# Optimization experiments

Measured on AMD Instinct MI355X. Metric: run time of the kernel, lower is better.

The kernel has to match this reference:

```python
import jax, jax.numpy as jnp
import numpy as np

B, P, K, HE, HF = 256, 128, 512, 1024, 512
D = K + HE + 2 * HF  # 2560, MLP input dim
HID = 64


def setup_inputs() -> dict:
    key = jax.random.key(0)
    ks = jax.random.split(key, 6)
    query = jax.random.normal(ks[0], (B, 1, HE), dtype=jnp.float32)
    keys = jax.random.normal(ks[1], (B, P, K), dtype=jnp.float32)
    frameLSTM_h = jax.random.normal(ks[2], (B, 1, 2 * HF), dtype=jnp.float32)
    mask = jax.random.randint(ks[3], (B, P), 0, 2, dtype=jnp.int32)
    mask = mask.at[:, 0].set(1)  # guarantee at least one unmasked player per row
    W1 = jax.random.normal(ks[4], (D, HID), dtype=jnp.float32) / np.float32(np.sqrt(D))
    W2 = jax.random.normal(ks[5], (HID, 1), dtype=jnp.float32) / np.float32(np.sqrt(HID))
    return dict(query=query, keys=keys, frameLSTM_h=frameLSTM_h, mask=mask, W1=W1, W2=W2)


def reference(query, keys, frameLSTM_h, mask, W1, W2):
    # Faithful to: cat([keys, query.repeat, frame.repeat]) @ W1 -> ReLU -> @ W2.
    # The pre-activation is linear, so splitting W1 by row-blocks is exactly the
    # same math without materializing the repeated/concatenated (B,P,D) tensor.
    W1k = W1[:K]            # (K, 64)
    W1q = W1[K:K + HE]      # (HE, 64)
    W1f = W1[K + HE:]       # (2*HF, 64)
    h = jax.nn.relu(
        jnp.einsum('bpk,kh->bph', keys, W1k)
        + jnp.einsum('boe,eh->boh', query, W1q)        # broadcasts over P
        + jnp.einsum('bof,fh->boh', frameLSTM_h, W1f)  # broadcasts over P
    )  # (B, P, 64)
    raw_scores = jnp.einsum('bph,ho->bp', h, W2)  # (B, P)
    raw_scores = jnp.where(mask == 0, -jnp.inf, raw_scores)
    weights = jax.nn.softmax(raw_scores, axis=1)  # (B, P)
    context = jnp.einsum('bp,bpk->bk', weights, keys)[:, None, :]  # (B, 1, K)
    embeddings = jnp.concatenate([context, frameLSTM_h], axis=2)   # (B, 1, K+2*HF)
    return embeddings, weights
```

## Files before the change

### kernel.cpp

```cpp
#include <hip/hip_runtime.h>
#include <hip/hip_bf16.h>
#include <cstdint>
#include <math.h>


typedef __bf16 bf16;
typedef __attribute__((ext_vector_type(8))) __bf16 bf16x8;
typedef __attribute__((ext_vector_type(4))) float f32x4;

#define NB 256
#define NP 128
#define NK 512

__global__ __launch_bounds__(512) void prep_kernel(
    const float* __restrict__ W1, const float* __restrict__ query,
    const float* __restrict__ frame, bf16* __restrict__ w1kt,
    float* __restrict__ proj)
{
    __shared__ float s[64][65];
    __shared__ float sq[4][2048];
    __shared__ float red[8][4][64];
    const int blk = blockIdx.x;
    const int t = threadIdx.x;
    if (blk < 8) {
        const int k0 = blk * 64;
#pragma unroll
        for (int i = 0; i < 8; i++) {
            const int idx = t + 512 * i;
            const int k = idx >> 6, h = idx & 63;
            s[k][h] = W1[(size_t)(k0 + k) * 64 + h];
        }
        __syncthreads();
#pragma unroll
        for (int i = 0; i < 8; i++) {
            const int idx = t + 512 * i;
            const int h = idx >> 6, kk = idx & 63;
            w1kt[(size_t)h * 512 + k0 + kk] = (bf16)s[kk][h];
        }
    } else {
        const int b0 = (blk - 8) * 4;
#pragma unroll
        for (int i = 0; i < 4; i++) {
            const int flat = (t + 512 * i) * 4;
            const int bl = flat >> 11;
            const int d  = flat & 2047;
            const float* src = (d < 1024)
                ? (query + (size_t)(b0 + bl) * 1024 + d)
                : (frame + (size_t)(b0 + bl) * 1024 + (d - 1024));
            *(float4*)&sq[bl][d] = *(const float4*)src;
        }
        __syncthreads();

        const int w = t >> 6;
        const int h = t & 63;
        const float* w1c = W1 + (size_t)(512 + w * 256) * 64 + h;
        float wreg[4][16];
#pragma unroll
        for (int bu = 0; bu < 3; bu++)
#pragma unroll
            for (int u = 0; u < 16; u++)
                wreg[bu][u] = w1c[(size_t)(bu * 16 + u) * 64];

        float acc[4] = {0.f, 0.f, 0.f, 0.f};
#pragma unroll
        for (int rr = 0; rr < 16; rr++) {
            const int cur = rr & 3;
            if (rr < 13) {
#pragma unroll
                for (int u = 0; u < 16; u++)
                    wreg[(rr + 3) & 3][u] = w1c[(size_t)((rr + 3) * 16 + u) * 64];
            }
#pragma unroll
            for (int u4 = 0; u4 < 4; u4++) {
                float4 qv[4];
#pragma unroll
                for (int j = 0; j < 4; j++)
                    qv[j] = *(const float4*)&sq[j][w * 256 + rr * 16 + u4 * 4];
#pragma unroll
                for (int uu = 0; uu < 4; uu++) {
                    const float wv = wreg[cur][u4 * 4 + uu];
                    acc[0] += (&qv[0].x)[uu] * wv;
                    acc[1] += (&qv[1].x)[uu] * wv;
                    acc[2] += (&qv[2].x)[uu] * wv;
                    acc[3] += (&qv[3].x)[uu] * wv;
                }
            }
        }
#pragma unroll
        for (int j = 0; j < 4; j++) red[w][j][h] = acc[j];
        __syncthreads();
        if (t < 256) {
            const int j2 = t >> 6, hh = t & 63;
            float sum = 0.f;
#pragma unroll
            for (int ww = 0; ww < 8; ww++) sum += red[ww][j2][hh];
            proj[(size_t)(b0 + j2) * 64 + hh] = sum;
        }
    }
}

__global__ __launch_bounds__(256) void scores_kernel(
    const float* __restrict__ keys, const float* __restrict__ W2,
    const bf16* __restrict__ w1kt, const float* __restrict__ proj,
    float* __restrict__ sws)
{
    extern __shared__ char sB[];
    const int blk = blockIdx.x;
    const int b = blk >> 1;
    const int ph = blk & 1;
    const int t = threadIdx.x;
    const int w = t >> 6;
    const int lane = t & 63;
    const int m = lane & 15;
    const int q = lane >> 4;
    const int p0 = ph * 64 + w * 16;
    const int xorv = (m & 7) << 4;

    const float* arow = keys + (size_t)b * (NP * NK) + (size_t)(p0 + m) * NK + q * 8;

    float4 Aa[4], Ab[4];
#pragma unroll
    for (int i = 0; i < 3; i++) {
        Aa[i] = *(const float4*)(arow + i * 32);
        Ab[i] = *(const float4*)(arow + i * 32 + 4);
    }

    {
        const char* wsrc = (const char*)w1kt;
#pragma unroll
        for (int i = 0; i < 16; i++) {
            const int o = t * 256 + i * 16;
            const int row = o >> 10;
            *(bf16x8*)(sB + (o ^ ((row & 7) << 4))) = *(const bf16x8*)(wsrc + o);
        }
    }

    float pv[4], wv[4];
#pragma unroll
    for (int nt = 0; nt < 4; nt++) {
        pv[nt] = proj[b * 64 + nt * 16 + m];
        wv[nt] = W2[nt * 16 + m];
    }
    __syncthreads();

    f32x4 acc[4];
#pragma unroll
    for (int nt = 0; nt < 4; nt++) acc[nt] = (f32x4){0.f, 0.f, 0.f, 0.f};

    bf16x8 Bp[2][4];
#pragma unroll
    for (int nt = 0; nt < 4; nt++)
        Bp[0][nt] = *(const bf16x8*)(sB + nt * 16384 + m * 1024 + ((q * 16) ^ xorv));

#pragma unroll
    for (int kk = 0; kk < 16; kk++) {
        const int cur = kk & 3;
        const int bc = kk & 1;
        if (kk < 13) {
            Aa[(kk + 3) & 3] = *(const float4*)(arow + (kk + 3) * 32);
            Ab[(kk + 3) & 3] = *(const float4*)(arow + (kk + 3) * 32 + 4);
        }
        if (kk < 15) {
#pragma unroll
            for (int nt = 0; nt < 4; nt++)
                Bp[bc ^ 1][nt] = *(const bf16x8*)(sB + nt * 16384 + m * 1024
                                  + ((((kk + 1) * 64) | (q * 16)) ^ xorv));
        }
        bf16x8 Af;
        Af[0] = (bf16)Aa[cur].x; Af[1] = (bf16)Aa[cur].y;
        Af[2] = (bf16)Aa[cur].z; Af[3] = (bf16)Aa[cur].w;
        Af[4] = (bf16)Ab[cur].x; Af[5] = (bf16)Ab[cur].y;
        Af[6] = (bf16)Ab[cur].z; Af[7] = (bf16)Ab[cur].w;
#pragma unroll
        for (int nt = 0; nt < 4; nt++)
            acc[nt] = __builtin_amdgcn_mfma_f32_16x16x32_bf16(Af, Bp[bc][nt], acc[nt], 0, 0, 0);
    }

    float pr[4] = {0.f, 0.f, 0.f, 0.f};
#pragma unroll
    for (int nt = 0; nt < 4; nt++)
#pragma unroll
        for (int r = 0; r < 4; r++)
            pr[r] += fmaxf(acc[nt][r] + pv[nt], 0.f) * wv[nt];

#pragma unroll
    for (int off = 1; off < 16; off <<= 1)
#pragma unroll
        for (int r = 0; r < 4; r++)
            pr[r] += __shfl_xor(pr[r], off);

    if (m == 0) {
#pragma unroll
        for (int r = 0; r < 4; r++)
            sws[(size_t)b * 128 + p0 + q * 4 + r] = pr[r];
    }
}

__global__ __launch_bounds__(512, 2) void ctx_kernel(
    const float* __restrict__ keys, const float* __restrict__ frame,
    const int* __restrict__ mask, const float* __restrict__ sws,
    float* __restrict__ out)
{
    __shared__ float wts[128];
    const int b = blockIdx.x;
    const int t = threadIdx.x;

    if (t < 64) {
        const int pa = t, pb = t + 64;
        float s0 = (mask[b * 128 + pa] == 0) ? -INFINITY : sws[(size_t)b * 128 + pa];
        float s1 = (mask[b * 128 + pb] == 0) ? -INFINITY : sws[(size_t)b * 128 + pb];
        float mx = fmaxf(s0, s1);
#pragma unroll
        for (int off = 32; off; off >>= 1) mx = fmaxf(mx, __shfl_xor(mx, off));
        float e0 = __expf(s0 - mx), e1 = __expf(s1 - mx);
        float sum = e0 + e1;
#pragma unroll
        for (int off = 32; off; off >>= 1) sum += __shfl_xor(sum, off);
        const float inv = 1.0f / sum;
        e0 *= inv; e1 *= inv;
        wts[pa] = e0; wts[pb] = e1;
        float* wout = out + (size_t)NB * 1536;
        wout[b * 128 + pa] = e0;
        wout[b * 128 + pb] = e1;
    }
    __syncthreads();

    const float* kc = keys + (size_t)b * (NP * NK) + t;
    float kreg[2][16];
#pragma unroll
    for (int i = 0; i < 16; i++) kreg[0][i] = kc[(size_t)i * NK];
    float acc = 0.f;
#pragma unroll
    for (int c8 = 0; c8 < 8; c8++) {
        const int cur = c8 & 1;
        if (c8 < 7) {
#pragma unroll
            for (int i = 0; i < 16; i++)
                kreg[cur ^ 1][i] = kc[(size_t)((c8 + 1) * 16 + i) * NK];
        }
#pragma unroll
        for (int i = 0; i < 16; i++)
            acc += wts[c8 * 16 + i] * kreg[cur][i];
    }
    out[(size_t)b * 1536 + t] = acc;

    if (t < 256) {
        const float4 fv = *(const float4*)(frame + (size_t)b * 1024 + t * 4);
        *(float4*)(out + (size_t)b * 1536 + 512 + t * 4) = fv;
    }
}

extern "C" void kernel_launch(void* const* d_in, const int* in_sizes, int n_in,
                              void* d_out, int out_size, void* d_ws, size_t ws_size,
                              hipStream_t stream) {
    const float* query = (const float*)d_in[0];
    const float* keys  = (const float*)d_in[1];
    const float* frame = (const float*)d_in[2];
    const int*   mask  = (const int*)d_in[3];
    const float* W1    = (const float*)d_in[4];
    const float* W2    = (const float*)d_in[5];
    float* out = (float*)d_out;

    bf16* w1kt  = (bf16*)d_ws;
    float* proj = (float*)((char*)d_ws + (64 << 10));
    float* sws  = (float*)((char*)d_ws + (128 << 10));

    hipFuncSetAttribute((const void*)scores_kernel,
                        hipFuncAttributeMaxDynamicSharedMemorySize, 65536);

    prep_kernel<<<72, 512, 0, stream>>>(W1, query, frame, w1kt, proj);
    scores_kernel<<<512, 256, 65536, stream>>>(keys, W2, w1kt, proj, sws);
    ctx_kernel<<<256, 512, 0, stream>>>(keys, frame, mask, sws, out);
}
```

Measured before the change: 130.6 us.

## Fuse scores and context kernels into one per-batch attention kernel

Merges the MFMA score kernel and the softmax/context kernel into a single kernel with one 512-thread block per batch row. Scores stay in shared memory instead of going through a global workspace, which removes one launch and the global round trip. The block also reads keys a second time while they may still be in L2. The key prefetch depth grows from 3 to 6 stages. The risks are that the grid drops to 256 blocks with more than 64KB of LDS each, which lowers occupancy and parallelism, and that the W1 tile load into LDS is now done once per batch rather than split across two blocks.

```diff
diff --git a/kernel.cpp b/kernel.cpp
--- a/kernel.cpp
+++ b/kernel.cpp
@@ -11,6 +11,7 @@
 #define NB 256
 #define NP 128
 #define NK 512
+#define SMEM_BYTES (65536 + 256 * 4)
 
 __global__ __launch_bounds__(512) void prep_kernel(
     const float* __restrict__ W1, const float* __restrict__ query,
@@ -99,28 +100,31 @@
     }
 }
 
-__global__ __launch_bounds__(256) void scores_kernel(
-    const float* __restrict__ keys, const float* __restrict__ W2,
+__global__ __launch_bounds__(512) void attn_kernel(
+    const float* __restrict__ keys, const float* __restrict__ frame,
+    const int* __restrict__ mask, const float* __restrict__ W2,
     const bf16* __restrict__ w1kt, const float* __restrict__ proj,
-    float* __restrict__ sws)
+    float* __restrict__ out)
 {
-    extern __shared__ char sB[];
-    const int blk = blockIdx.x;
-    const int b = blk >> 1;
-    const int ph = blk & 1;
+    extern __shared__ char smem[];
+    char* sB      = smem;
+    float* scores = (float*)(smem + 65536);
+    float* wts    = scores + 128;
+
+    const int b = blockIdx.x;
     const int t = threadIdx.x;
     const int w = t >> 6;
     const int lane = t & 63;
     const int m = lane & 15;
     const int q = lane >> 4;
-    const int p0 = ph * 64 + w * 16;
+    const int p0 = w * 16;
     const int xorv = (m & 7) << 4;
 
     const float* arow = keys + (size_t)b * (NP * NK) + (size_t)(p0 + m) * NK + q * 8;
 
-    float4 Aa[4], Ab[4];
-#pragma unroll
-    for (int i = 0; i < 3; i++) {
+    float4 Aa[8], Ab[8];
+#pragma unroll
+    for (int i = 0; i < 6; i++) {
         Aa[i] = *(const float4*)(arow + i * 32);
         Ab[i] = *(const float4*)(arow + i * 32 + 4);
     }
@@ -128,8 +132,8 @@
     {
         const char* wsrc = (const char*)w1kt;
 #pragma unroll
-        for (int i = 0; i < 16; i++) {
-            const int o = t * 256 + i * 16;
+        for (int i = 0; i < 8; i++) {
+            const int o = i * 8192 + t * 16;
             const int row = o >> 10;
             *(bf16x8*)(sB + (o ^ ((row & 7) << 4))) = *(const bf16x8*)(wsrc + o);
         }
@@ -154,11 +158,11 @@
 
 #pragma unroll
     for (int kk = 0; kk < 16; kk++) {
-        const int cur = kk & 3;
+        const int cur = kk & 7;
         const int bc = kk & 1;
-        if (kk < 13) {
-            Aa[(kk + 3) & 3] = *(const float4*)(arow + (kk + 3) * 32);
-            Ab[(kk + 3) & 3] = *(const float4*)(arow + (kk + 3) * 32 + 4);
+        if (kk < 10) {
+            Aa[(kk + 6) & 7] = *(const float4*)(arow + (kk + 6) * 32);
+            Ab[(kk + 6) & 7] = *(const float4*)(arow + (kk + 6) * 32 + 4);
         }
         if (kk < 15) {
 #pragma unroll
@@ -191,24 +195,14 @@
 
     if (m == 0) {
 #pragma unroll
-        for (int r = 0; r < 4; r++)
-            sws[(size_t)b * 128 + p0 + q * 4 + r] = pr[r];
-    }
-}
-
-__global__ __launch_bounds__(512, 2) void ctx_kernel(
-    const float* __restrict__ keys, const float* __restrict__ frame,
-    const int* __restrict__ mask, const float* __restrict__ sws,
-    float* __restrict__ out)
-{
-    __shared__ float wts[128];
-    const int b = blockIdx.x;
-    const int t = threadIdx.x;
+        for (int r = 0; r < 4; r++) scores[p0 + q * 4 + r] = pr[r];
+    }
+    __syncthreads();
 
     if (t < 64) {
         const int pa = t, pb = t + 64;
-        float s0 = (mask[b * 128 + pa] == 0) ? -INFINITY : sws[(size_t)b * 128 + pa];
-        float s1 = (mask[b * 128 + pb] == 0) ? -INFINITY : sws[(size_t)b * 128 + pb];
+        float s0 = (mask[b * 128 + pa] == 0) ? -INFINITY : scores[pa];
+        float s1 = (mask[b * 128 + pb] == 0) ? -INFINITY : scores[pb];
         float mx = fmaxf(s0, s1);
 #pragma unroll
         for (int off = 32; off; off >>= 1) mx = fmaxf(mx, __shfl_xor(mx, off));
@@ -225,25 +219,26 @@
     }
     __syncthreads();
 
-    const float* kc = keys + (size_t)b * (NP * NK) + t;
-    float kreg[2][16];
-#pragma unroll
-    for (int i = 0; i < 16; i++) kreg[0][i] = kc[(size_t)i * NK];
-    float acc = 0.f;
-#pragma unroll
-    for (int c8 = 0; c8 < 8; c8++) {
-        const int cur = c8 & 1;
-        if (c8 < 7) {
+    {
+        const float* kc = keys + (size_t)b * (NP * NK) + t;
+        float kreg[2][16];
+#pragma unroll
+        for (int i = 0; i < 16; i++) kreg[0][i] = kc[(size_t)i * NK];
+        float acc2 = 0.f;
+#pragma unroll
+        for (int c8 = 0; c8 < 8; c8++) {
+            const int cu2 = c8 & 1;
+            if (c8 < 7) {
+#pragma unroll
+                for (int i = 0; i < 16; i++)
+                    kreg[cu2 ^ 1][i] = kc[(size_t)((c8 + 1) * 16 + i) * NK];
+            }
 #pragma unroll
             for (int i = 0; i < 16; i++)
-                kreg[cur ^ 1][i] = kc[(size_t)((c8 + 1) * 16 + i) * NK];
-        }
-#pragma unroll
-        for (int i = 0; i < 16; i++)
-            acc += wts[c8 * 16 + i] * kreg[cur][i];
-    }
-    out[(size_t)b * 1536 + t] = acc;
-
+                acc2 += wts[c8 * 16 + i] * kreg[cu2][i];
+        }
+        out[(size_t)b * 1536 + t] = acc2;
+    }
     if (t < 256) {
         const float4 fv = *(const float4*)(frame + (size_t)b * 1024 + t * 4);
         *(float4*)(out + (size_t)b * 1536 + 512 + t * 4) = fv;
@@ -263,12 +258,11 @@
 
     bf16* w1kt  = (bf16*)d_ws;
     float* proj = (float*)((char*)d_ws + (64 << 10));
-    float* sws  = (float*)((char*)d_ws + (128 << 10));
-
-    hipFuncSetAttribute((const void*)scores_kernel,
-                        hipFuncAttributeMaxDynamicSharedMemorySize, 65536);
+
+    hipFuncSetAttribute((const void*)attn_kernel,
+                        hipFuncAttributeMaxDynamicSharedMemorySize, SMEM_BYTES);
 
     prep_kernel<<<72, 512, 0, stream>>>(W1, query, frame, w1kt, proj);
-    scores_kernel<<<512, 256, 65536, stream>>>(keys, W2, w1kt, proj, sws);
-    ctx_kernel<<<256, 512, 0, stream>>>(keys, frame, mask, sws, out);
+    attn_kernel<<<256, 512, SMEM_BYTES, stream>>>(keys, frame, mask, W2,
+                                                  w1kt, proj, out);
 }
```

New measurement: 123.6 us. -5.4%, faster.
